# Kernel tuning notes

Measured on AMD Instinct MI355X. Metric: run time of the kernel, lower is better.

## Reference

```python
import jax, jax.numpy as jnp
import numpy as np

N_HEAD, D_K, D_V, EPS = 8, 64, 64, 1e-6


def setup_inputs() -> dict:
    key = jax.random.key(0)
    ks = jax.random.split(key, 7)
    b, n, t, d = 8, 4, 512, 512
    q = jax.random.normal(ks[0], (b, n, t, d), dtype=jnp.float32)
    k = jax.random.normal(ks[1], (b, n, t, d), dtype=jnp.float32)
    v = jax.random.normal(ks[2], (b, n, t, d), dtype=jnp.float32)
    s = 1.0 / np.sqrt(d)
    w_q = jax.random.normal(ks[3], (N_HEAD * D_K, d), dtype=jnp.float32) * s
    w_k = jax.random.normal(ks[4], (N_HEAD * D_K, d), dtype=jnp.float32) * s
    w_v = jax.random.normal(ks[5], (N_HEAD * D_V, d), dtype=jnp.float32) * s
    w_fc = jax.random.normal(ks[6], (d, N_HEAD * D_V), dtype=jnp.float32) * s
    ln_gamma = jnp.ones((d,), dtype=jnp.float32)
    ln_beta = jnp.zeros((d,), dtype=jnp.float32)
    return {"q": q, "k": k, "v": v, "w_q": w_q, "w_k": w_k, "w_v": w_v,
            "w_fc": w_fc, "ln_gamma": ln_gamma, "ln_beta": ln_beta}


def reference(q, k, v, w_q, w_k, w_v, w_fc, ln_gamma, ln_beta):
    b, n, t, d = q.shape
    B = b * n
    qf = q.reshape(B, t, d)
    kf = k.reshape(B, t, d)
    vf = v.reshape(B, t, d)
    residual = qf
    # projections -> [B, H, T, dk/dv]
    Q = jnp.einsum('btd,ed->bte', qf, w_q).reshape(B, t, N_HEAD, D_K).transpose(0, 2, 1, 3)
    K = jnp.einsum('btd,ed->bte', kf, w_k).reshape(B, t, N_HEAD, D_K).transpose(0, 2, 1, 3)
    V = jnp.einsum('btd,ed->bte', vf, w_v).reshape(B, t, N_HEAD, D_V).transpose(0, 2, 1, 3)
    # scaled dot-product attention (scale by sqrt(d_k) of q's last dim)
    scale = 1.0 / jnp.sqrt(jnp.asarray(D_K, dtype=Q.dtype))
    attn = jax.nn.softmax(jnp.einsum('bhqd,bhkd->bhqk', Q * scale, K), axis=-1)
    O = jnp.einsum('bhqk,bhkd->bhqd', attn, V)  # [B, H, T, dv]
    # merge heads, then the original's extra transpose+view (layout scramble)
    x = O.transpose(0, 2, 1, 3).reshape(B, t, N_HEAD * D_V)
    x = jnp.transpose(x, (0, 2, 1)).reshape(B, t, N_HEAD * D_V)
    x = jnp.einsum('bte,de->btd', x, w_fc)
    x = x + residual
    # LayerNorm(eps=1e-6)
    mu = jnp.mean(x, axis=-1, keepdims=True)
    var = jnp.var(x, axis=-1, keepdims=True)
    x = (x - mu) * jax.lax.rsqrt(var + EPS) * ln_gamma + ln_beta
    return x.reshape(b, n, t, d)
```

## Files before the change

kernel.cpp:

```cpp
#include <hip/hip_runtime.h>
#include <hip/hip_bf16.h>
#include <stdint.h>

typedef __attribute__((ext_vector_type(8))) short bf16x8;
typedef __attribute__((ext_vector_type(4))) float f32x4;
typedef __attribute__((ext_vector_type(16))) float f32x16;
typedef unsigned int u32;

#define MFMA16(a,b,c) __builtin_amdgcn_mfma_f32_16x16x32_bf16((a),(b),(c),0,0,0)
#define MFMA32(a,b,c) __builtin_amdgcn_mfma_f32_32x32x16_bf16((a),(b),(c),0,0,0)

__device__ __forceinline__ unsigned short f2bf(float f) {
    unsigned u = __float_as_uint(f);
    u = (u + 0x7FFFu + ((u >> 16) & 1u)) >> 16;
    return (unsigned short)u;
}
__device__ __forceinline__ float bf2f(unsigned short h) {
    return __uint_as_float(((unsigned)h) << 16);
}
__device__ __forceinline__ u32 cvt_pk_bf16(float lo, float hi) {
    u32 r;
    asm("v_cvt_pk_bf16_f32 %0, %1, %2" : "=v"(r) : "v"(lo), "v"(hi));
    return r;
}
__device__ __forceinline__ void gload16(const unsigned short* gp, unsigned short* lp) {
    __builtin_amdgcn_global_load_lds(
        (const __attribute__((address_space(1))) u32*)gp,
        (__attribute__((address_space(3))) u32*)lp, 16, 0, 0);
}
__device__ __forceinline__ int xcd_swz(int bid, int q8) {
    return (bid & 7) * q8 + (bid >> 3);
}


__global__ __launch_bounds__(256) void prep_kernel(
    const float* __restrict__ q, const float* __restrict__ k, const float* __restrict__ v,
    const float* __restrict__ wq, const float* __restrict__ wk, const float* __restrict__ wv,
    const float* __restrict__ wfc,
    unsigned short* __restrict__ Xq, unsigned short* __restrict__ Xk, unsigned short* __restrict__ Xv,
    unsigned short* __restrict__ Wcat)
{
    const long c = (long)blockIdx.x * 256 + threadIdx.x;
    const float* src;
    unsigned short* dst;
    long off;
    if (c < 3145728) {
        const int t = (int)(c >> 20);
        off = (c & 1048575) * 8;
        src = (t == 0) ? q : (t == 1) ? k : v;
        dst = (t == 0) ? Xq : (t == 1) ? Xk : Xv;
    } else {
        const long c2 = c - 3145728;
        const int w = (int)(c2 >> 15);
        off = (c2 & 32767) * 8;
        src = (w == 0) ? wq : (w == 1) ? wk : (w == 2) ? wv : wfc;
        dst = Wcat + (long)w * 262144;
    }
    const float4 a = *(const float4*)(src + off);
    const float4 b = *(const float4*)(src + off + 4);
    uint4 pk;
    pk.x = (u32)f2bf(a.x) | ((u32)f2bf(a.y) << 16);
    pk.y = (u32)f2bf(a.z) | ((u32)f2bf(a.w) << 16);
    pk.z = (u32)f2bf(b.x) | ((u32)f2bf(b.y) << 16);
    pk.w = (u32)f2bf(b.z) | ((u32)f2bf(b.w) << 16);
    *(uint4*)(dst + off) = pk;
}

__device__ __forceinline__ void gemm_body(
    const unsigned short* __restrict__ A, const unsigned short* __restrict__ Bm,
    unsigned short* __restrict__ out, int mode, float scale,
    unsigned short* As0, unsigned short* Bs0,
    unsigned short* As1, unsigned short* Bs1,
    int m0, int n0)
{
    const int tid = threadIdx.x, wid = tid >> 6, lane = tid & 63;
    const int wm = wid >> 1, wn = wid & 1;
    const int g = lane >> 4, cc = lane & 15;

    f32x4 acc[4][4];
    #pragma unroll
    for (int a = 0; a < 4; a++)
        #pragma unroll
        for (int b = 0; b < 4; b++)
            acc[a][b] = (f32x4){0.f, 0.f, 0.f, 0.f};

    auto STAGE = [&](unsigned short* As, unsigned short* Bs, int k0) {
        #pragma unroll
        for (int j = 0; j < 4; j++) {
            const int sb = j * 256 + wid * 64;
            const int s = sb + lane;
            const int r = s >> 3;
            const int cd = (s & 7) ^ (r & 7);
            gload16(A  + (size_t)(m0 + r) * 512 + k0 + cd * 8, As + (size_t)sb * 8);
            gload16(Bm + (size_t)(n0 + r) * 512 + k0 + cd * 8, Bs + (size_t)sb * 8);
        }
    };

    STAGE(As0, Bs0, 0);
    __syncthreads();

    #pragma unroll
    for (int t = 0; t < 8; t++) {
        unsigned short* Ac = (t & 1) ? As1 : As0;
        unsigned short* Bc = (t & 1) ? Bs1 : Bs0;
        if (t < 7)
            STAGE((t & 1) ? As0 : As1, (t & 1) ? Bs0 : Bs1, (t + 1) * 64);

        #pragma unroll
        for (int kc = 0; kc < 2; kc++) {
            bf16x8 af[4], bfr[4];
            #pragma unroll
            for (int mf = 0; mf < 4; mf++) {
                const int r = wm * 64 + mf * 16 + cc;
                af[mf] = *(const bf16x8*)(Ac + r * 64 + (((kc * 4 + g) ^ (r & 7)) * 8));
            }
            #pragma unroll
            for (int nf = 0; nf < 4; nf++) {
                const int r = wn * 64 + nf * 16 + cc;
                bfr[nf] = *(const bf16x8*)(Bc + r * 64 + (((kc * 4 + g) ^ (r & 7)) * 8));
            }
            __builtin_amdgcn_s_setprio(1);
            #pragma unroll
            for (int mf = 0; mf < 4; mf++)
                #pragma unroll
                for (int nf = 0; nf < 4; nf++)
                    acc[mf][nf] = MFMA16(af[mf], bfr[nf], acc[mf][nf]);
            __builtin_amdgcn_s_setprio(0);
        }
        __syncthreads();
    }

    #pragma unroll
    for (int mf = 0; mf < 4; mf++) {
        const int rg = m0 + wm * 64 + mf * 16 + g * 4;
        const int t0 = rg & 511, bI = rg >> 9;
        #pragma unroll
        for (int nf = 0; nf < 4; nf++) {
            const int col = n0 + wn * 64 + nf * 16 + cc;
            if (mode == 0) {
                const int h = col >> 6, dd = col & 63;
                const size_t base = ((size_t)((bI * 8 + h) * 512 + t0)) * 64 + dd;
                #pragma unroll
                for (int i = 0; i < 4; i++)
                    out[base + (size_t)i * 64] = f2bf(acc[mf][nf][i] * scale);
            } else if (mode == 1) {
                const int h = col >> 6, dd = col & 63;
                const size_t base = ((size_t)((bI * 8 + h) * 64 + dd)) * 512 + t0;
                uint2 pk;
                pk.x = (u32)f2bf(acc[mf][nf][0]) | ((u32)f2bf(acc[mf][nf][1]) << 16);
                pk.y = (u32)f2bf(acc[mf][nf][2]) | ((u32)f2bf(acc[mf][nf][3]) << 16);
                *(uint2*)(out + base) = pk;
            } else {
                #pragma unroll
                for (int i = 0; i < 4; i++)
                    out[(size_t)(rg + i) * 512 + col] = f2bf(acc[mf][nf][i]);
            }
        }
    }
}

__global__ __launch_bounds__(256) void proj_kernel(
    const unsigned short* __restrict__ Xq, const unsigned short* __restrict__ Xk,
    const unsigned short* __restrict__ Xv, const unsigned short* __restrict__ Wcat,
    unsigned short* __restrict__ Qb, unsigned short* __restrict__ Kb,
    unsigned short* __restrict__ Vt)
{
    __shared__ __align__(16) unsigned short As[2][128 * 64];
    __shared__ __align__(16) unsigned short Bs[2][128 * 64];
    const int work = xcd_swz(blockIdx.x, 192);
    const int x = work & 3, y = (work >> 2) & 127, z = work >> 9;
    const unsigned short* A = (z == 0) ? Xq : (z == 1) ? Xk : Xv;
    const unsigned short* B = Wcat + (size_t)z * 262144;
    unsigned short* out = (z == 0) ? Qb : (z == 1) ? Kb : Vt;
    const int mode = (z == 2) ? 1 : 0;
    const float scale = (z == 0) ? 0.125f : 1.0f;
    gemm_body(A, B, out, mode, scale, As[0], Bs[0], As[1], Bs[1], y * 128, x * 128);
}

__global__ __launch_bounds__(256) void fc_kernel(
    const unsigned short* __restrict__ Os, const unsigned short* __restrict__ Wfc,
    unsigned short* __restrict__ Y)
{
    __shared__ __align__(16) unsigned short As[2][128 * 64];
    __shared__ __align__(16) unsigned short Bs[2][128 * 64];
    const int work = xcd_swz(blockIdx.x, 64);
    const int x = work & 3, y = work >> 2;
    gemm_body(Os, Wfc, Y, 2, 1.0f, As[0], Bs[0], As[1], Bs[1], y * 128, x * 128);
}

__global__ __launch_bounds__(256) void attn_kernel(
    const unsigned short* __restrict__ Qb, const unsigned short* __restrict__ Kb,
    const unsigned short* __restrict__ Vt, unsigned short* __restrict__ Os)
{
    __shared__ __align__(16) unsigned short Ks[64 * 64];
    __shared__ __align__(16) unsigned short Vs[64 * 64];

    const int work = xcd_swz(blockIdx.x, 128);
    const int qt = work & 3, bh = work >> 2;
    const int tid = threadIdx.x;
    const int wid = tid >> 6, lane = tid & 63;
    const int l31 = lane & 31, hi = lane >> 5;

    const unsigned short* Qp = Qb + (size_t)bh * 512 * 64;
    const unsigned short* Kp = Kb + (size_t)bh * 512 * 64;
    const unsigned short* Vp = Vt + (size_t)bh * 64 * 512;

    const int q0 = qt * 128 + wid * 32;

    bf16x8 qf[4];
    #pragma unroll
    for (int c = 0; c < 4; c++)
        qf[c] = *(const bf16x8*)(Qp + (size_t)(q0 + l31) * 64 + c * 16 + hi * 8);

    f32x16 o0, o1;
    #pragma unroll
    for (int r = 0; r < 16; r++) { o0[r] = 0.f; o1[r] = 0.f; }
    float lrun = 0.f;

    const int sb = wid * 64;
    const int s1 = sb + lane, r1 = s1 >> 3, cd1 = (s1 & 7) ^ (r1 & 7);
    const int s2 = sb + 256 + lane, r2 = s2 >> 3, cd2 = (s2 & 7) ^ (r2 & 7);

    const int swz0 = l31 & 7;

    for (int kt = 0; kt < 8; kt++) {
        gload16(Kp + (size_t)(kt * 64 + r1) * 64 + cd1 * 8, Ks + (size_t)sb * 8);
        gload16(Kp + (size_t)(kt * 64 + r2) * 64 + cd2 * 8, Ks + (size_t)(sb + 256) * 8);
        gload16(Vp + (size_t)r1 * 512 + kt * 64 + cd1 * 8, Vs + (size_t)sb * 8);
        gload16(Vp + (size_t)r2 * 512 + kt * 64 + cd2 * 8, Vs + (size_t)(sb + 256) * 8);
        __syncthreads();

        f32x16 sT0, sT1;
        #pragma unroll
        for (int r = 0; r < 16; r++) { sT0[r] = 0.f; sT1[r] = 0.f; }
        __builtin_amdgcn_s_setprio(1);
        #pragma unroll
        for (int c = 0; c < 4; c++) {
            const int cs = c * 2 + hi;
            bf16x8 kf0 = *(const bf16x8*)(Ks + l31 * 64 + ((cs ^ swz0) * 8));
            bf16x8 kf1 = *(const bf16x8*)(Ks + (32 + l31) * 64 + ((cs ^ swz0) * 8));
            sT0 = MFMA32(kf0, qf[c], sT0);
            sT1 = MFMA32(kf1, qf[c], sT1);
        }
        __builtin_amdgcn_s_setprio(0);

        u32 wA[8], wB[8];
        #pragma unroll
        for (int j = 0; j < 8; j++) {
            float a0 = __expf(sT0[2 * j]), a1 = __expf(sT0[2 * j + 1]);
            float b0 = __expf(sT1[2 * j]), b1 = __expf(sT1[2 * j + 1]);
            lrun += (a0 + a1) + (b0 + b1);
            wA[j] = cvt_pk_bf16(a0, a1);
            wB[j] = cvt_pk_bf16(b0, b1);
        }
        #pragma unroll
        for (int jb = 0; jb < 8; jb += 4) {
            asm("v_permlane32_swap_b32 %0, %1" : "+v"(wA[jb + 0]), "+v"(wA[jb + 2]));
            asm("v_permlane32_swap_b32 %0, %1" : "+v"(wA[jb + 1]), "+v"(wA[jb + 3]));
            asm("v_permlane32_swap_b32 %0, %1" : "+v"(wB[jb + 0]), "+v"(wB[jb + 2]));
            asm("v_permlane32_swap_b32 %0, %1" : "+v"(wB[jb + 1]), "+v"(wB[jb + 3]));
        }

        __builtin_amdgcn_s_setprio(1);
        #pragma unroll
        for (int ck = 0; ck < 4; ck++) {
            const u32* w = (ck < 2) ? wA : wB;
            const int jb = (ck & 1) * 4;
            union { u32 u[4]; bf16x8 v; } pa;
            pa.u[0] = w[jb + 0];
            pa.u[1] = w[jb + 1];
            pa.u[2] = w[jb + 2];
            pa.u[3] = w[jb + 3];
            const int cs = ck * 2 + hi;
            bf16x8 vb0 = *(const bf16x8*)(Vs + l31 * 64 + ((cs ^ swz0) * 8));
            bf16x8 vb1 = *(const bf16x8*)(Vs + (32 + l31) * 64 + ((cs ^ swz0) * 8));
            o0 = MFMA32(pa.v, vb0, o0);
            o1 = MFMA32(pa.v, vb1, o1);
        }
        __builtin_amdgcn_s_setprio(0);
        __syncthreads();
    }

    const float lsum = lrun + __shfl_xor(lrun, 32);
    const float inv = 1.0f / lsum;
    float iv[16];
    #pragma unroll
    for (int qd = 0; qd < 4; qd++)
        #pragma unroll
        for (int i = 0; i < 4; i++)
            iv[qd * 4 + i] = __shfl(inv, qd * 8 + 4 * hi + i);

    const int b = bh >> 3, h = bh & 7;
    #pragma unroll
    for (int dvt = 0; dvt < 2; dvt++) {
        const f32x16& o = dvt ? o1 : o0;
        const int dv = dvt * 32 + l31;
        const size_t rowbase = ((size_t)b * 512 + h * 64 + dv) * 512;
        #pragma unroll
        for (int qd = 0; qd < 4; qd++) {
            uint2 pk;
            pk.x = cvt_pk_bf16(o[qd * 4 + 0] * iv[qd * 4 + 0], o[qd * 4 + 1] * iv[qd * 4 + 1]);
            pk.y = cvt_pk_bf16(o[qd * 4 + 2] * iv[qd * 4 + 2], o[qd * 4 + 3] * iv[qd * 4 + 3]);
            *(uint2*)(Os + rowbase + q0 + qd * 8 + 4 * hi) = pk;
        }
    }
}

__global__ __launch_bounds__(256) void ln_kernel(
    const unsigned short* __restrict__ y, const unsigned short* __restrict__ residb,
    const float* __restrict__ gamma, const float* __restrict__ beta,
    float* __restrict__ out)
{
    const int wid = threadIdx.x >> 6, lane = threadIdx.x & 63;
    const int row = blockIdx.x * 4 + wid;

    const bf16x8 yv = *(const bf16x8*)(y + (size_t)row * 512 + lane * 8);
    const bf16x8 rv = *(const bf16x8*)(residb + (size_t)row * 512 + lane * 8);
    float x[8];
    #pragma unroll
    for (int j = 0; j < 8; j++)
        x[j] = bf2f((unsigned short)yv[j]) + bf2f((unsigned short)rv[j]);

    float s = 0.f, sq = 0.f;
    #pragma unroll
    for (int j = 0; j < 8; j++) { s += x[j]; sq += x[j] * x[j]; }
    #pragma unroll
    for (int d = 1; d < 64; d <<= 1) {
        s += __shfl_xor(s, d);
        sq += __shfl_xor(sq, d);
    }
    const float mu = s * (1.0f / 512.0f);
    const float var = sq * (1.0f / 512.0f) - mu * mu;
    const float rs = rsqrtf(var + 1e-6f);

    #pragma unroll
    for (int j = 0; j < 2; j++) {
        const int colb = lane * 8 + j * 4;
        const float4 gg = *(const float4*)(gamma + colb);
        const float4 bb = *(const float4*)(beta + colb);
        float4 ov;
        ov.x = (x[j * 4 + 0] - mu) * rs * gg.x + bb.x;
        ov.y = (x[j * 4 + 1] - mu) * rs * gg.y + bb.y;
        ov.z = (x[j * 4 + 2] - mu) * rs * gg.z + bb.z;
        ov.w = (x[j * 4 + 3] - mu) * rs * gg.w + bb.w;
        *(float4*)(out + (size_t)row * 512 + colb) = ov;
    }
}

extern "C" void kernel_launch(void* const* d_in, const int* in_sizes, int n_in,
                              void* d_out, int out_size, void* d_ws, size_t ws_size,
                              hipStream_t stream) {
    const float* q     = (const float*)d_in[0];
    const float* k     = (const float*)d_in[1];
    const float* v     = (const float*)d_in[2];
    const float* wq    = (const float*)d_in[3];
    const float* wk    = (const float*)d_in[4];
    const float* wv    = (const float*)d_in[5];
    const float* wfc   = (const float*)d_in[6];
    const float* gamma = (const float*)d_in[7];
    const float* beta  = (const float*)d_in[8];
    float* out = (float*)d_out;

    char* ws = (char*)d_ws;
    const size_t SEG = 16777216;
    unsigned short* Xq   = (unsigned short*)(ws);
    unsigned short* Xk   = (unsigned short*)(ws + SEG);
    unsigned short* Xv   = (unsigned short*)(ws + 2 * SEG);
    unsigned short* Qb   = (unsigned short*)(ws + 3 * SEG);
    unsigned short* Kb   = (unsigned short*)(ws + 4 * SEG);
    unsigned short* Vt   = (unsigned short*)(ws + 5 * SEG);
    unsigned short* Wcat = (unsigned short*)(ws + 6 * SEG);
    unsigned short* Os = Xv;
    unsigned short* Y  = Xk;

    prep_kernel<<<12800, 256, 0, stream>>>(q, k, v, wq, wk, wv, wfc, Xq, Xk, Xv, Wcat);
    proj_kernel<<<1536, 256, 0, stream>>>(Xq, Xk, Xv, Wcat, Qb, Kb, Vt);
    attn_kernel<<<1024, 256, 0, stream>>>(Qb, Kb, Vt, Os);
    fc_kernel<<<512, 256, 0, stream>>>(Os, Wcat + 786432, Y);
    ln_kernel<<<4096, 256, 0, stream>>>(Y, Xq, gamma, beta, out);
}
```

Before: 120.4 us.

## Load GEMM A operand directly from global into registers, bypassing LDS

The shared GEMM body now reads A-operand MFMA fragments straight from global memory into double-buffered registers instead of staging them through LDS. Only the B tile stays in shared memory, which halves LDS use per block and removes the LDS write/read traffic for A. The cost is that each wave (two waves share each A row block) issues its own uncoalesced-ish 16-byte global loads for A. It also adds register pressure from the two register buffers of A fragments, which could reduce occupancy or expose global latency.

```diff
diff --git a/kernel.cpp b/kernel.cpp
--- a/kernel.cpp
+++ b/kernel.cpp
@@ -69,8 +69,7 @@
 __device__ __forceinline__ void gemm_body(
     const unsigned short* __restrict__ A, const unsigned short* __restrict__ Bm,
     unsigned short* __restrict__ out, int mode, float scale,
-    unsigned short* As0, unsigned short* Bs0,
-    unsigned short* As1, unsigned short* Bs1,
+    unsigned short* Bs0, unsigned short* Bs1,
     int m0, int n0)
 {
     const int tid = threadIdx.x, wid = tid >> 6, lane = tid & 63;
@@ -84,36 +83,44 @@
         for (int b = 0; b < 4; b++)
             acc[a][b] = (f32x4){0.f, 0.f, 0.f, 0.f};
 
-    auto STAGE = [&](unsigned short* As, unsigned short* Bs, int k0) {
+    auto STAGEB = [&](unsigned short* Bs, int k0) {
         #pragma unroll
         for (int j = 0; j < 4; j++) {
             const int sb = j * 256 + wid * 64;
             const int s = sb + lane;
             const int r = s >> 3;
             const int cd = (s & 7) ^ (r & 7);
-            gload16(A  + (size_t)(m0 + r) * 512 + k0 + cd * 8, As + (size_t)sb * 8);
             gload16(Bm + (size_t)(n0 + r) * 512 + k0 + cd * 8, Bs + (size_t)sb * 8);
         }
     };
-
-    STAGE(As0, Bs0, 0);
+    const unsigned short* Arow = A + (size_t)(m0 + wm * 64 + cc) * 512 + g * 8;
+    auto LOADA = [&](bf16x8 (&af)[4][2], int k0) {
+        #pragma unroll
+        for (int mf = 0; mf < 4; mf++)
+            #pragma unroll
+            for (int kc = 0; kc < 2; kc++)
+                af[mf][kc] = *(const bf16x8*)(Arow + (size_t)(mf * 16) * 512 + k0 + kc * 32);
+    };
+
+    bf16x8 aA[4][2], aB[4][2];
+    LOADA(aA, 0);
+    STAGEB(Bs0, 0);
     __syncthreads();
 
     #pragma unroll
     for (int t = 0; t < 8; t++) {
-        unsigned short* Ac = (t & 1) ? As1 : As0;
+        auto& acur = (t & 1) ? aB : aA;
+        auto& anext = (t & 1) ? aA : aB;
         unsigned short* Bc = (t & 1) ? Bs1 : Bs0;
-        if (t < 7)
-            STAGE((t & 1) ? As0 : As1, (t & 1) ? Bs0 : Bs1, (t + 1) * 64);
+        unsigned short* Bn = (t & 1) ? Bs0 : Bs1;
+        if (t < 7) {
+            LOADA(anext, (t + 1) * 64);
+            STAGEB(Bn, (t + 1) * 64);
+        }
 
         #pragma unroll
         for (int kc = 0; kc < 2; kc++) {
-            bf16x8 af[4], bfr[4];
-            #pragma unroll
-            for (int mf = 0; mf < 4; mf++) {
-                const int r = wm * 64 + mf * 16 + cc;
-                af[mf] = *(const bf16x8*)(Ac + r * 64 + (((kc * 4 + g) ^ (r & 7)) * 8));
-            }
+            bf16x8 bfr[4];
             #pragma unroll
             for (int nf = 0; nf < 4; nf++) {
                 const int r = wn * 64 + nf * 16 + cc;
@@ -124,7 +131,7 @@
             for (int mf = 0; mf < 4; mf++)
                 #pragma unroll
                 for (int nf = 0; nf < 4; nf++)
-                    acc[mf][nf] = MFMA16(af[mf], bfr[nf], acc[mf][nf]);
+                    acc[mf][nf] = MFMA16(acur[mf][kc], bfr[nf], acc[mf][nf]);
             __builtin_amdgcn_s_setprio(0);
         }
         __syncthreads();
@@ -165,7 +172,6 @@
     unsigned short* __restrict__ Qb, unsigned short* __restrict__ Kb,
     unsigned short* __restrict__ Vt)
 {
-    __shared__ __align__(16) unsigned short As[2][128 * 64];
     __shared__ __align__(16) unsigned short Bs[2][128 * 64];
     const int work = xcd_swz(blockIdx.x, 192);
     const int x = work & 3, y = (work >> 2) & 127, z = work >> 9;
@@ -174,18 +180,17 @@
     unsigned short* out = (z == 0) ? Qb : (z == 1) ? Kb : Vt;
     const int mode = (z == 2) ? 1 : 0;
     const float scale = (z == 0) ? 0.125f : 1.0f;
-    gemm_body(A, B, out, mode, scale, As[0], Bs[0], As[1], Bs[1], y * 128, x * 128);
+    gemm_body(A, B, out, mode, scale, Bs[0], Bs[1], y * 128, x * 128);
 }
 
 __global__ __launch_bounds__(256) void fc_kernel(
     const unsigned short* __restrict__ Os, const unsigned short* __restrict__ Wfc,
     unsigned short* __restrict__ Y)
 {
-    __shared__ __align__(16) unsigned short As[2][128 * 64];
     __shared__ __align__(16) unsigned short Bs[2][128 * 64];
     const int work = xcd_swz(blockIdx.x, 64);
     const int x = work & 3, y = work >> 2;
-    gemm_body(Os, Wfc, Y, 2, 1.0f, As[0], Bs[0], As[1], Bs[1], y * 128, x * 128);
+    gemm_body(Os, Wfc, Y, 2, 1.0f, Bs[0], Bs[1], y * 128, x * 128);
 }
 
 __global__ __launch_bounds__(256) void attn_kernel(
```

After: 153.6 us. 27.6% more time.
